# Performance work log

Measured on AMD Instinct MI355X. Metric: run time of the kernel, lower is better.

The kernel has to match this reference:

```python
import jax, jax.numpy as jnp
import numpy as np

A_BITS = 3
W_BITS = 3

def setup_inputs() -> dict:
    key = jax.random.key(0)
    k1, k2 = jax.random.split(key)
    # activations: small nonnegative ints (will be clipped to [0, 2^A_bits-1])
    x = jax.random.randint(k1, (32, 256, 56, 56), 0, 2 ** A_BITS, dtype=jnp.int32)
    # weights: torch.randint(0, 2**W_bits - 1, ...) -> values in [0, 6]
    weight = jax.random.randint(k2, (256, 256, 3, 3), 0, 2 ** W_BITS - 1).astype(jnp.float32)
    return {"x": x, "weight": weight}

def reference(x, weight):
    # quantize: clip activations to [0, 2^A_bits - 1]; truncate weight to int
    xq = jnp.clip(x.astype(jnp.int32), 0, 2 ** A_BITS - 1).astype(jnp.float32)
    wq = weight.astype(jnp.int32).astype(jnp.float32)  # OIHW, nonneg small ints
    # direct conv2d, stride 1, no padding (VALID). Small ints -> exact in fp32.
    out = jax.lax.conv_general_dilated(
        xq, wq,
        window_strides=(1, 1),
        padding="VALID",
        dimension_numbers=("NCHW", "OIHW", "NCHW"),
    )
    return out  # [32, 256, 54, 54]
```

## Files before the change

### kernel.cpp

```cpp
#include <hip/hip_runtime.h>
#include <stdint.h>

typedef int i32x4 __attribute__((ext_vector_type(4)));
typedef float f32x4 __attribute__((ext_vector_type(4)));

#define N_IMG 32
#define C_IN 256
#define H_IN 56
#define W_IN 56
#define K_OUT 256
#define H_OUT 54
#define W_OUT 54
#define HW_OUT 2916
#define M_PIX 93312
#define CHW_OUT 746496

#define BM 192

#define XT_BYTES ((size_t)N_IMG * H_IN * W_IN * C_IN)
#define WT_BYTES ((size_t)9 * K_OUT * C_IN)

__global__ __launch_bounds__(256) void xform(const int* __restrict__ x,
                                             const float* __restrict__ w,
                                             unsigned char* __restrict__ xt,
                                             unsigned char* __restrict__ wt) {
    const int bid = blockIdx.x;
    if (bid < N_IMG * H_IN) {
        const int n = bid / H_IN;
        const int h = bid % H_IN;
        const int c = threadIdx.x;
        const int* src = x + ((size_t)((n * C_IN + c) * H_IN + h)) * W_IN;
        unsigned char* dst = xt + ((size_t)(n * H_IN + h) * W_IN) * C_IN + c;
        #pragma unroll
        for (int w0 = 0; w0 < W_IN; w0 += 4) {
            int4 v = *(const int4*)(src + w0);
            int a[4] = {v.x, v.y, v.z, v.w};
            #pragma unroll
            for (int j = 0; j < 4; ++j) {
                int q = a[j] < 0 ? 0 : (a[j] > 7 ? 7 : a[j]);
                dst[(size_t)(w0 + j) * C_IN] = (unsigned char)q;
            }
        }
    } else {
        const int o = bid - N_IMG * H_IN;
        const int c = threadIdx.x;
        const float* src = w + ((size_t)o * C_IN + c) * 9;
        const int h  = c >> 7;
        const int kk = (c >> 6) & 1;
        const int g  = (c >> 4) & 3;
        const int b  = c & 15;
        #pragma unroll
        for (int rs = 0; rs < 9; ++rs) {
            int iv = (int)src[rs];
            wt[(size_t)((rs * 2 + h) * 2 + kk) * 16384 + o * 64 + g * 16 + b]
                = (unsigned char)iv;
        }
    }
}

__device__ __forceinline__ void gload_lds16(const void* g, void* l) {
    __builtin_amdgcn_global_load_lds(
        (const __attribute__((address_space(1))) uint32_t*)g,
        (__attribute__((address_space(3))) uint32_t*)l,
        16, 0, 0);
}

__global__ __launch_bounds__(512, 2) void conv_mfma(const unsigned char* __restrict__ xt,
                                                    const unsigned char* __restrict__ wt,
                                                    float* __restrict__ out) {
    __shared__ __align__(16) unsigned char halo[57344];

    const int t512 = threadIdx.x;
    const int l    = t512 & 63;
    const int wid  = t512 >> 6;
    const int wr   = wid >> 2;
    const int wc   = wid & 3;
    const int mb   = blockIdx.x;

    const int slot = t512 & 7;
    const int srow = t512 >> 3;
    const int cs   = ((slot ^ (srow & 7)) << 4);
    const int tb16 = t512 * 16;
    const int sb   = srow * 256 + cs;

    const int m0  = mb * BM;
    const int n0  = m0 / HW_OUT;
    const int rm0 = m0 - n0 * HW_OUT;
    const int oh0 = rm0 / W_OUT;
    const int ow0 = rm0 - oh0 * W_OUT;
    const int pix0 = n0 * (H_IN * W_IN) + oh0 * W_IN + ow0;

    const int lrow = l & 15;
    int drow[6];
    #pragma unroll
    for (int mf = 0; mf < 6; ++mf) {
        const int m   = m0 + wr * 96 + mf * 16 + lrow;
        const int n   = m / HW_OUT;
        const int rem = m - n * HW_OUT;
        const int oh  = rem / W_OUT;
        const int ow  = rem - oh * W_OUT;
        drow[mf] = n * (H_IN * W_IN) + oh * W_IN + ow - pix0;
    }

    const unsigned g16 = (unsigned)((l >> 4) << 4);

    const char* wb = (const char*)wt;
    const char* bptr[4];
    #pragma unroll
    for (int nf = 0; nf < 4; ++nf)
        bptr[nf] = wb + (wc * 64 + nf * 16 + (l & 15)) * 64 + (l >> 4) * 16;

    i32x4 acc[6][4];
    #pragma unroll
    for (int i = 0; i < 6; ++i)
        #pragma unroll
        for (int j = 0; j < 4; ++j)
            acc[i][j] = (i32x4){0, 0, 0, 0};

    const char* xb = (const char*)xt;

    #define STAGE_HALO(H) do {                                               \
        const char* hs_ = xb + (size_t)pix0 * 256 + (H) * 128 + sb;          \
        _Pragma("unroll")                                                    \
        for (int i_ = 0; i_ < 7; ++i_)                                       \
            gload_lds16(hs_ + (size_t)i_ * 16384, halo + i_ * 8192 + tb16);  \
    } while (0)

    #define LOADB(B, TAP, H) do {                                            \
        const int bo_ = ((TAP) * 2 + (H)) * 32768;                           \
        _Pragma("unroll")                                                    \
        for (int nf = 0; nf < 4; ++nf) {                                     \
            B[nf][0] = *(const i32x4*)(bptr[nf] + bo_);                      \
            B[nf][1] = *(const i32x4*)(bptr[nf] + bo_ + 16384);              \
        }                                                                    \
    } while (0)

    #define TILE(B, TAP) do {                                                \
        const int toff_ = ((TAP) / 3) * W_IN + ((TAP) % 3);                  \
        _Pragma("unroll")                                                    \
        for (int kk = 0; kk < 2; ++kk) {                                     \
            i32x4 av_[6];                                                    \
            _Pragma("unroll")                                                \
            for (int mf = 0; mf < 6; ++mf) {                                 \
                const int row_ = drow[mf] + toff_;                           \
                const unsigned off_ = ((unsigned)row_ << 7) +                \
                    (((unsigned)(kk << 6) + g16) ^ ((unsigned)(row_ & 7) << 4)); \
                av_[mf] = *(const i32x4*)(halo + off_);                      \
            }                                                                \
            _Pragma("unroll")                                                \
            for (int mf = 0; mf < 6; ++mf)                                   \
                _Pragma("unroll")                                            \
                for (int nf = 0; nf < 4; ++nf)                               \
                    acc[mf][nf] = __builtin_amdgcn_mfma_i32_16x16x64_i8(     \
                        av_[mf], B[nf][kk], acc[mf][nf], 0, 0, 0);           \
        }                                                                    \
    } while (0)

    i32x4 b0[4][2], b1[4][2];

    STAGE_HALO(0);
    LOADB(b0, 0, 0);
    asm volatile("s_waitcnt vmcnt(0)" ::: "memory");
    __builtin_amdgcn_s_barrier();

    #pragma unroll
    for (int t = 0; t < 8; t += 2) {
        LOADB(b1, t + 1, 0);
        TILE(b0, t);
        LOADB(b0, t + 2, 0);
        TILE(b1, t + 1);
    }
    LOADB(b1, 0, 1);
    TILE(b0, 8);

    __builtin_amdgcn_s_barrier();
    STAGE_HALO(1);
    asm volatile("s_waitcnt vmcnt(0)" ::: "memory");
    __builtin_amdgcn_s_barrier();

    #pragma unroll
    for (int t = 0; t < 8; t += 2) {
        LOADB(b0, t + 1, 1);
        TILE(b1, t);
        LOADB(b1, t + 2, 1);
        TILE(b0, t + 1);
    }
    TILE(b1, 8);

    const int c16 = l & 15;
    const int p4  = (l >> 4) << 2;
    #pragma unroll
    for (int mf = 0; mf < 6; ++mf) {
        const int m   = mb * BM + wr * 96 + mf * 16 + p4;
        const int n   = m / HW_OUT;
        const int rem = m - n * HW_OUT;
        float* ob = out + (size_t)n * CHW_OUT + rem;
        #pragma unroll
        for (int nf = 0; nf < 4; ++nf) {
            const int ch = wc * 64 + nf * 16 + c16;
            f32x4 v;
            #pragma unroll
            for (int j = 0; j < 4; ++j) v[j] = (float)acc[mf][nf][j];
            *(f32x4*)(ob + (size_t)ch * HW_OUT) = v;
        }
    }
    #undef TILE
    #undef LOADB
    #undef STAGE_HALO
}

__global__ __launch_bounds__(256) void conv_naive(const int* __restrict__ x,
                                                  const float* __restrict__ w,
                                                  float* __restrict__ out) {
    int idx = blockIdx.x * 256 + threadIdx.x;
    if (idx >= N_IMG * K_OUT * HW_OUT) return;
    const int wo = idx % W_OUT;
    int tmp = idx / W_OUT;
    const int ho = tmp % H_OUT; tmp /= H_OUT;
    const int k = tmp % K_OUT;
    const int n = tmp / K_OUT;
    float acc = 0.f;
    for (int c = 0; c < C_IN; ++c) {
        const int* xp = x + ((size_t)((n * C_IN + c) * H_IN + ho)) * W_IN + wo;
        const float* wp = w + ((size_t)(k * C_IN + c)) * 9;
        #pragma unroll
        for (int r = 0; r < 3; ++r)
            #pragma unroll
            for (int s = 0; s < 3; ++s) {
                int xv = xp[r * W_IN + s];
                xv = xv < 0 ? 0 : (xv > 7 ? 7 : xv);
                acc += (float)xv * (float)(int)wp[r * 3 + s];
            }
    }
    out[idx] = acc;
}

extern "C" void kernel_launch(void* const* d_in, const int* in_sizes, int n_in,
                              void* d_out, int out_size, void* d_ws, size_t ws_size,
                              hipStream_t stream) {
    const int*   x = (const int*)d_in[0];
    const float* w = (const float*)d_in[1];
    float* out = (float*)d_out;

    const size_t need = XT_BYTES + WT_BYTES;
    if (ws_size >= need) {
        unsigned char* xt = (unsigned char*)d_ws;
        unsigned char* wt = (unsigned char*)((char*)d_ws + XT_BYTES);
        hipLaunchKernelGGL(xform, dim3(N_IMG * H_IN + K_OUT), dim3(256), 0, stream,
                           x, w, xt, wt);
        hipLaunchKernelGGL(conv_mfma, dim3(M_PIX / BM), dim3(512), 0, stream,
                           xt, wt, out);
    } else {
        const int total = N_IMG * K_OUT * HW_OUT;
        hipLaunchKernelGGL(conv_naive, dim3((total + 255) / 256), dim3(256), 0, stream, x, w, out);
    }
}
```

Before: 94.72 us.

## Double-buffer LDS A-fragments across taps and raise MFMA wave priority

Restructures the per-tap loop so the LDS reads of the A fragments for the next tap are issued before the MFMAs of the current tap, using two register buffers (av0/av1) alongside the existing B double buffer. Each block of 48 MFMAs is wrapped in s_setprio(1)/s_setprio(0) so matrix work gets issue priority over other waves. The aim is to hide LDS read latency behind matrix work. In exchange it roughly doubles A-fragment register use, which risks lower occupancy or spills.

Result: slower. 184.0 us (+94.3%).

```diff
diff --git a/kernel.cpp b/kernel.cpp
--- a/kernel.cpp
+++ b/kernel.cpp
@@ -135,57 +135,66 @@
         }                                                                    \
     } while (0)
 
-    #define TILE(B, TAP) do {                                                \
+    #define DSREAD_AV(AV, TAP) do {                                          \
         const int toff_ = ((TAP) / 3) * W_IN + ((TAP) % 3);                  \
         _Pragma("unroll")                                                    \
-        for (int kk = 0; kk < 2; ++kk) {                                     \
-            i32x4 av_[6];                                                    \
-            _Pragma("unroll")                                                \
-            for (int mf = 0; mf < 6; ++mf) {                                 \
-                const int row_ = drow[mf] + toff_;                           \
-                const unsigned off_ = ((unsigned)row_ << 7) +                \
-                    (((unsigned)(kk << 6) + g16) ^ ((unsigned)(row_ & 7) << 4)); \
-                av_[mf] = *(const i32x4*)(halo + off_);                      \
-            }                                                                \
+        for (int mf = 0; mf < 6; ++mf) {                                     \
+            const int row_ = drow[mf] + toff_;                               \
+            const unsigned rb_ = ((unsigned)row_ << 7);                      \
+            const unsigned sw_ = ((unsigned)(row_ & 7)) << 4;                \
+            AV[mf][0] = *(const i32x4*)(halo + rb_ + (g16 ^ sw_));           \
+            AV[mf][1] = *(const i32x4*)(halo + rb_ + ((64u + g16) ^ sw_));   \
+        }                                                                    \
+    } while (0)
+
+    #define MFMA48(AV, B) do {                                               \
+        __builtin_amdgcn_s_setprio(1);                                       \
+        _Pragma("unroll")                                                    \
+        for (int kk = 0; kk < 2; ++kk)                                       \
             _Pragma("unroll")                                                \
             for (int mf = 0; mf < 6; ++mf)                                   \
                 _Pragma("unroll")                                            \
                 for (int nf = 0; nf < 4; ++nf)                               \
                     acc[mf][nf] = __builtin_amdgcn_mfma_i32_16x16x64_i8(     \
-                        av_[mf], B[nf][kk], acc[mf][nf], 0, 0, 0);           \
+                        AV[mf][kk], B[nf][kk], acc[mf][nf], 0, 0, 0);        \
+        __builtin_amdgcn_s_setprio(0);                                       \
+    } while (0)
+
+    #define RUN_HALF(H, P) do {                                              \
+        _Pragma("unroll")                                                    \
+        for (int t = 0; t < 9; ++t) {                                        \
+            if (t < 8) {                                                     \
+                if ((((t + (P) + 1) & 1)) == 0) { LOADB(b0, t + 1, (H)); }   \
+                else                            { LOADB(b1, t + 1, (H)); }   \
+            } else if ((H) == 0) {                                           \
+                LOADB(b1, 0, 1);      \
+            }                                                                \
+            if (t < 8) {                                                     \
+                if ((((t + (P) + 1) & 1)) == 0) { DSREAD_AV(av0, t + 1); }   \
+                else                            { DSREAD_AV(av1, t + 1); }   \
+            }                                                                \
+            if ((((t + (P)) & 1)) == 0) { MFMA48(av0, b0); }                 \
+            else                        { MFMA48(av1, b1); }                 \
         }                                                                    \
     } while (0)
 
-    i32x4 b0[4][2], b1[4][2];
+    i32x4 av0[6][2], av1[6][2], b0[4][2], b1[4][2];
 
     STAGE_HALO(0);
     LOADB(b0, 0, 0);
     asm volatile("s_waitcnt vmcnt(0)" ::: "memory");
     __builtin_amdgcn_s_barrier();
-
-    #pragma unroll
-    for (int t = 0; t < 8; t += 2) {
-        LOADB(b1, t + 1, 0);
-        TILE(b0, t);
-        LOADB(b0, t + 2, 0);
-        TILE(b1, t + 1);
-    }
-    LOADB(b1, 0, 1);
-    TILE(b0, 8);
+    DSREAD_AV(av0, 0);
+
+    RUN_HALF(0, 0);
 
     __builtin_amdgcn_s_barrier();
     STAGE_HALO(1);
     asm volatile("s_waitcnt vmcnt(0)" ::: "memory");
     __builtin_amdgcn_s_barrier();
-
-    #pragma unroll
-    for (int t = 0; t < 8; t += 2) {
-        LOADB(b0, t + 1, 1);
-        TILE(b1, t);
-        LOADB(b1, t + 2, 1);
-        TILE(b0, t + 1);
-    }
-    TILE(b1, 8);
+    DSREAD_AV(av1, 0);
+
+    RUN_HALF(1, 1);
 
     const int c16 = l & 15;
     const int p4  = (l >> 4) << 2;
@@ -204,7 +213,9 @@
             *(f32x4*)(ob + (size_t)ch * HW_OUT) = v;
         }
     }
-    #undef TILE
+    #undef RUN_HALF
+    #undef MFMA48
+    #undef DSREAD_AV
     #undef LOADB
     #undef STAGE_HALO
 }
```

## Shrink M tile to 128 and raise occupancy with smaller halo and single B buffer

Applied to the files above, without the earlier changes.

Reduces the per-block pixel tile from 192 to 128, shrinking the LDS halo buffer to 368 rows and the accumulator array to 4x4. Launch bounds move to 4 blocks per CU, and the double-buffered B registers become a single buffer loaded after each tap's MFMAs. It also wraps the MFMA bursts in s_setprio. The aim is more resident waves to hide latency, paid for with more halo overlap per output and less register prefetching of B.

After: 192.6 us. 103% more time.

```diff
diff --git a/kernel.cpp b/kernel.cpp
--- a/kernel.cpp
+++ b/kernel.cpp
@@ -15,7 +15,8 @@
 #define M_PIX 93312
 #define CHW_OUT 746496
 
-#define BM 192
+#define BM 128
+#define HALO_ROWS 368
 
 #define XT_BYTES ((size_t)N_IMG * H_IN * W_IN * C_IN)
 #define WT_BYTES ((size_t)9 * K_OUT * C_IN)
@@ -65,10 +66,10 @@
         16, 0, 0);
 }
 
-__global__ __launch_bounds__(512, 2) void conv_mfma(const unsigned char* __restrict__ xt,
+__global__ __launch_bounds__(512, 4) void conv_mfma(const unsigned char* __restrict__ xt,
                                                     const unsigned char* __restrict__ wt,
                                                     float* __restrict__ out) {
-    __shared__ __align__(16) unsigned char halo[57344];
+    __shared__ __align__(16) unsigned char halo[HALO_ROWS * 128];
 
     const int t512 = threadIdx.x;
     const int l    = t512 & 63;
@@ -91,10 +92,10 @@
     const int pix0 = n0 * (H_IN * W_IN) + oh0 * W_IN + ow0;
 
     const int lrow = l & 15;
-    int drow[6];
-    #pragma unroll
-    for (int mf = 0; mf < 6; ++mf) {
-        const int m   = m0 + wr * 96 + mf * 16 + lrow;
+    int drow[4];
+    #pragma unroll
+    for (int mf = 0; mf < 4; ++mf) {
+        const int m   = m0 + wr * 64 + mf * 16 + lrow;
         const int n   = m / HW_OUT;
         const int rem = m - n * HW_OUT;
         const int oh  = rem / W_OUT;
@@ -110,9 +111,9 @@
     for (int nf = 0; nf < 4; ++nf)
         bptr[nf] = wb + (wc * 64 + nf * 16 + (l & 15)) * 64 + (l >> 4) * 16;
 
-    i32x4 acc[6][4];
-    #pragma unroll
-    for (int i = 0; i < 6; ++i)
+    i32x4 acc[4][4];
+    #pragma unroll
+    for (int i = 0; i < 4; ++i)
         #pragma unroll
         for (int j = 0; j < 4; ++j)
             acc[i][j] = (i32x4){0, 0, 0, 0};
@@ -122,56 +123,55 @@
     #define STAGE_HALO(H) do {                                               \
         const char* hs_ = xb + (size_t)pix0 * 256 + (H) * 128 + sb;          \
         _Pragma("unroll")                                                    \
-        for (int i_ = 0; i_ < 7; ++i_)                                       \
+        for (int i_ = 0; i_ < 5; ++i_)                                       \
             gload_lds16(hs_ + (size_t)i_ * 16384, halo + i_ * 8192 + tb16);  \
+        if (t512 < 384)                                                      \
+            gload_lds16(hs_ + (size_t)5 * 16384, halo + 5 * 8192 + tb16);    \
     } while (0)
 
-    #define LOADB(B, TAP, H) do {                                            \
+    #define LOADB(TAP, H) do {                                               \
         const int bo_ = ((TAP) * 2 + (H)) * 32768;                           \
         _Pragma("unroll")                                                    \
         for (int nf = 0; nf < 4; ++nf) {                                     \
-            B[nf][0] = *(const i32x4*)(bptr[nf] + bo_);                      \
-            B[nf][1] = *(const i32x4*)(bptr[nf] + bo_ + 16384);              \
+            bv[nf][0] = *(const i32x4*)(bptr[nf] + bo_);                     \
+            bv[nf][1] = *(const i32x4*)(bptr[nf] + bo_ + 16384);             \
         }                                                                    \
     } while (0)
 
-    #define TILE(B, TAP) do {                                                \
+    #define STEP(TAP, LB_TAP, LB_H, DO_LB) do {                              \
         const int toff_ = ((TAP) / 3) * W_IN + ((TAP) % 3);                  \
+        i32x4 av_[4];                                                        \
         _Pragma("unroll")                                                    \
         for (int kk = 0; kk < 2; ++kk) {                                     \
-            i32x4 av_[6];                                                    \
             _Pragma("unroll")                                                \
-            for (int mf = 0; mf < 6; ++mf) {                                 \
+            for (int mf = 0; mf < 4; ++mf) {                                 \
                 const int row_ = drow[mf] + toff_;                           \
                 const unsigned off_ = ((unsigned)row_ << 7) +                \
                     (((unsigned)(kk << 6) + g16) ^ ((unsigned)(row_ & 7) << 4)); \
                 av_[mf] = *(const i32x4*)(halo + off_);                      \
             }                                                                \
+            __builtin_amdgcn_s_setprio(1);                                   \
             _Pragma("unroll")                                                \
-            for (int mf = 0; mf < 6; ++mf)                                   \
+            for (int mf = 0; mf < 4; ++mf)                                   \
                 _Pragma("unroll")                                            \
                 for (int nf = 0; nf < 4; ++nf)                               \
                     acc[mf][nf] = __builtin_amdgcn_mfma_i32_16x16x64_i8(     \
-                        av_[mf], B[nf][kk], acc[mf][nf], 0, 0, 0);           \
+                        av_[mf], bv[nf][kk], acc[mf][nf], 0, 0, 0);          \
+            __builtin_amdgcn_s_setprio(0);                                   \
         }                                                                    \
+        if (DO_LB) LOADB(LB_TAP, LB_H);                                      \
     } while (0)
 
-    i32x4 b0[4][2], b1[4][2];
+    i32x4 bv[4][2];
 
     STAGE_HALO(0);
-    LOADB(b0, 0, 0);
+    LOADB(0, 0);
     asm volatile("s_waitcnt vmcnt(0)" ::: "memory");
     __builtin_amdgcn_s_barrier();
 
     #pragma unroll
-    for (int t = 0; t < 8; t += 2) {
-        LOADB(b1, t + 1, 0);
-        TILE(b0, t);
-        LOADB(b0, t + 2, 0);
-        TILE(b1, t + 1);
-    }
-    LOADB(b1, 0, 1);
-    TILE(b0, 8);
+    for (int t = 0; t < 8; ++t) STEP(t, t + 1, 0, 1);
+    STEP(8, 0, 1, 1);
 
     __builtin_amdgcn_s_barrier();
     STAGE_HALO(1);
@@ -179,19 +179,14 @@
     __builtin_amdgcn_s_barrier();
 
     #pragma unroll
-    for (int t = 0; t < 8; t += 2) {
-        LOADB(b0, t + 1, 1);
-        TILE(b1, t);
-        LOADB(b1, t + 2, 1);
-        TILE(b0, t + 1);
-    }
-    TILE(b1, 8);
+    for (int t = 0; t < 8; ++t) STEP(t, t + 1, 1, 1);
+    STEP(8, 0, 0, 0);
 
     const int c16 = l & 15;
     const int p4  = (l >> 4) << 2;
     #pragma unroll
-    for (int mf = 0; mf < 6; ++mf) {
-        const int m   = mb * BM + wr * 96 + mf * 16 + p4;
+    for (int mf = 0; mf < 4; ++mf) {
+        const int m   = mb * BM + wr * 64 + mf * 16 + p4;
         const int n   = m / HW_OUT;
         const int rem = m - n * HW_OUT;
         float* ob = out + (size_t)n * CHW_OUT + rem;
@@ -204,7 +199,7 @@
             *(f32x4*)(ob + (size_t)ch * HW_OUT) = v;
         }
     }
-    #undef TILE
+    #undef STEP
     #undef LOADB
     #undef STAGE_HALO
 }
```
